# Optimization experiments

Measured on AMD Instinct MI355X. Metric: run time of the kernel, lower is better.

The kernel has to match this reference:

```python
import jax, jax.numpy as jnp
import numpy as np

N = 26000       # total nodes (1040 graphs * 25 joints)
E = 208000      # total edges
G = 1040        # graphs (16 samples * 65 frames)
FRAMES = 65
F_IN = 6
HID = 128
HEADS = 4
NCLS = 7


def setup_inputs() -> dict:
    key = jax.random.key(0)
    ks = jax.random.split(key, 30)

    def nrm(k, shape, s=0.05):
        return jax.random.normal(k, shape, dtype=jnp.float32) * s

    return {
        "x": jax.random.normal(ks[0], (N, F_IN), dtype=jnp.float32),
        "edge_index": jax.random.randint(ks[1], (2, E), 0, N, dtype=jnp.int32),
        "batch": jnp.arange(N, dtype=jnp.int32) // (N // G),  # 25 nodes per graph
        "w1_root": nrm(ks[2], (F_IN, HID)),
        "w1_nei": nrm(ks[3], (F_IN, HID)),
        "b1": nrm(ks[4], (HID,)),
        "wq": nrm(ks[5], (HID, HEADS * HID)),
        "bq": nrm(ks[6], (HEADS * HID,)),
        "wk": nrm(ks[7], (HID, HEADS * HID)),
        "bk": nrm(ks[8], (HEADS * HID,)),
        "wv": nrm(ks[9], (HID, HEADS * HID)),
        "bv": nrm(ks[10], (HEADS * HID,)),
        "wskip": nrm(ks[11], (HID, HEADS * HID)),
        "bskip": nrm(ks[12], (HEADS * HID,)),
        "skip_w": nrm(ks[13], (HID, HEADS * HID)),
        "lin1_w": nrm(ks[14], (HEADS * HID, HID)),
        "lin1_b": nrm(ks[15], (HID,)),
        "l2_root": nrm(ks[16], (HID, HID)),
        "l2_nei": nrm(ks[17], (HID, HID)),
        "l2_b": nrm(ks[18], (HID,)),
        "l3_root": nrm(ks[19], (HID, HID)),
        "l3_nei": nrm(ks[20], (HID, HID)),
        "l3_b": nrm(ks[21], (HID,)),
        "fc_w": nrm(ks[22], (HID, NCLS)),
        "fc_b": nrm(ks[23], (NCLS,)),
    }


def _graph_conv(x, src, dst, w_root, w_nei, b):
    # PyG GraphConv (aggr='add'): W_root x_i + W_nei * sum_{j in N(i)} x_j + b
    agg = jax.ops.segment_sum(x[src], dst, num_segments=N)
    return x @ w_root + agg @ w_nei + b


def _transformer_conv(x, src, dst, wq, bq, wk, bk, wv, bv, wskip, bskip):
    # PyG TransformerConv, concat=True, root_weight=True, beta=False.
    # Dropout on attention is inference-disabled.
    q = (x @ wq + bq).reshape(N, HEADS, HID)
    k = (x @ wk + bk).reshape(N, HEADS, HID)
    v = (x @ wv + bv).reshape(N, HEADS, HID)
    logits = jnp.einsum('ehc,ehc->eh', q[dst], k[src]) / jnp.sqrt(jnp.float32(HID))
    m = jax.ops.segment_max(logits, dst, num_segments=N)          # [N,H]
    a = jnp.exp(logits - m[dst])                                  # [E,H]
    denom = jax.ops.segment_sum(a, dst, num_segments=N)           # [N,H]
    num = jax.ops.segment_sum(a[:, :, None] * v[src], dst, num_segments=N)  # [N,H,C]
    out = num / jnp.where(denom == 0, 1.0, denom)[:, :, None]
    return out.reshape(N, HEADS * HID) + (x @ wskip + bskip)


def reference(x, edge_index, batch,
              w1_root, w1_nei, b1,
              wq, bq, wk, bk, wv, bv, wskip, bskip,
              skip_w, lin1_w, lin1_b,
              l2_root, l2_nei, l2_b,
              l3_root, l3_nei, l3_b,
              fc_w, fc_b):
    src, dst = edge_index[0], edge_index[1]
    h = jax.nn.relu(_graph_conv(x, src, dst, w1_root, w1_nei, b1))
    skip_out = h @ skip_w  # external skip Linear (no bias)
    h = jax.nn.relu(_transformer_conv(h, src, dst, wq, bq, wk, bk, wv, bv, wskip, bskip) + skip_out)
    h = jax.nn.relu(h @ lin1_w + lin1_b)
    for wr, wn, b in ((l2_root, l2_nei, l2_b), (l3_root, l3_nei, l3_b)):
        h = jax.nn.relu(_graph_conv(h, src, dst, wr, wn, b) + h)
    # global_mean_pool over graphs
    sums = jax.ops.segment_sum(h, batch, num_segments=G)
    cnts = jax.ops.segment_sum(jnp.ones((N,), jnp.float32), batch, num_segments=G)
    pooled = sums / jnp.where(cnts == 0, 1.0, cnts)[:, None]      # [G, HID]
    # average over 65 frames per sample, then classify
    z = pooled.reshape(-1, FRAMES, HID).mean(axis=1)              # [G/65, HID]
    return z @ fc_w + fc_b
```

## Files before the change

### kernel.cpp

```cpp
#include <hip/hip_runtime.h>
#include <math.h>

#define NN 26000
#define NE 208000
#define SCAN_CH 26

typedef __attribute__((ext_vector_type(8))) short bf16x8;
typedef __attribute__((ext_vector_type(4))) float f32x4;
typedef __attribute__((ext_vector_type(2))) float f32x2;
typedef unsigned char u8;

__device__ __forceinline__ float bf2f(ushort u){
  union { unsigned int i; float f; } w; w.i = ((unsigned int)u) << 16; return w.f;
}
__device__ __forceinline__ ushort f2bf(float f){
  union { float f; unsigned int i; } w; w.f = f;
  unsigned int u = w.i + 0x7fffu + ((w.i >> 16) & 1u);
  return (ushort)(u >> 16);
}

__global__ void count_k(const int* __restrict__ dst, int* __restrict__ cnt, int E){
  int e = blockIdx.x*256 + threadIdx.x;
  if (e < E) atomicAdd(&cnt[dst[e]], 1);
}

__global__ __launch_bounds__(1024) void scan_k(int* __restrict__ cnt_cur, int* __restrict__ off){
  int t = threadIdx.x;
  int base = t * SCAN_CH;
  int v[SCAN_CH];
  #pragma unroll
  for (int j = 0; j < SCAN_CH; ++j){
    int idx = base + j;
    v[j] = (idx < NN) ? cnt_cur[idx] : 0;
  }
  int s = 0;
  #pragma unroll
  for (int j = 0; j < SCAN_CH; ++j) s += v[j];
  __shared__ int ls[1024];
  ls[t] = s; __syncthreads();
  for (int ofs = 1; ofs < 1024; ofs <<= 1){
    int u = (t >= ofs) ? ls[t - ofs] : 0;
    __syncthreads();
    ls[t] += u;
    __syncthreads();
  }
  int run = (t == 0) ? 0 : ls[t-1];
  #pragma unroll
  for (int j = 0; j < SCAN_CH; ++j){
    int idx = base + j;
    if (idx < NN){
      off[idx] = run;
      cnt_cur[idx] = run;
      run += v[j];
    }
  }
  if (t == 1023) off[NN] = ls[1023];
}

__global__ void fill_k(const int* __restrict__ src, const int* __restrict__ dst,
                       int* __restrict__ cur, int* __restrict__ csrc, int E){
  int e = blockIdx.x*256 + threadIdx.x;
  if (e < E){
    int p = atomicAdd(&cur[dst[e]], 1);
    csrc[p] = src[e];
  }
}

__global__ __launch_bounds__(256) void layer1_k(
    const float* __restrict__ x, const int* __restrict__ off,
    const int* __restrict__ csrc, const float* __restrict__ w1r,
    const float* __restrict__ w1n, const float* __restrict__ b1,
    ushort* __restrict__ h1)
{
  __shared__ float aggs[2][6];
  int slot = threadIdx.x >> 7, c = threadIdx.x & 127;
  int i = blockIdx.x*2 + slot;
  if (c < 6){
    float s = 0.f;
    int e1 = off[i+1];
    for (int j = off[i]; j < e1; ++j) s += x[(size_t)csrc[j]*6 + c];
    aggs[slot][c] = s;
  }
  __syncthreads();
  float s = b1[c];
  #pragma unroll
  for (int f = 0; f < 6; ++f){
    s = fmaf(x[i*6+f],    w1r[f*128+c], s);
    s = fmaf(aggs[slot][f], w1n[f*128+c], s);
  }
  h1[(size_t)i*128 + c] = f2bf(fmaxf(s, 0.f));
}

__global__ void prep_w(const float* __restrict__ wq, const float* __restrict__ wk,
                       const float* __restrict__ wv, const float* __restrict__ wskip,
                       const float* __restrict__ skw, const float* __restrict__ lin1w,
                       const float* __restrict__ l2r, const float* __restrict__ l2n,
                       const float* __restrict__ l3r, const float* __restrict__ l3n,
                       ushort* __restrict__ wbuf){
  int idx = blockIdx.x*256 + threadIdx.x;
  if (idx >= 393216) return;
  float v;
  if (idx < 262144){
    int seg = idx >> 16;
    int local = idx & 65535;
    int n = local >> 7, kk = local & 127;
    const float* w = (seg == 0) ? wq : (seg == 1) ? wk : (seg == 2) ? wv : wskip;
    v = w[kk*512 + n];
    if (seg == 3) v += skw[kk*512 + n];
  } else if (idx < 327680){
    int local = idx - 262144;
    int n = local >> 9, kk = local & 511;
    v = lin1w[kk*128 + n];
  } else {
    int rem = idx - 327680;
    int seg = rem >> 14;
    int local = rem & 16383;
    int n = local >> 7, kk = local & 127;
    const float* w = (seg == 0) ? l2r : (seg == 1) ? l2n : (seg == 2) ? l3r : l3n;
    v = w[kk*128 + n];
  }
  wbuf[idx] = f2bf(v);
}

__global__ __launch_bounds__(256) void qkvs_k(
    const ushort* __restrict__ A, const ushort* __restrict__ BT,
    const float* __restrict__ bq, const float* __restrict__ bk,
    const float* __restrict__ bv, const float* __restrict__ bs,
    ushort* __restrict__ cq, u8* __restrict__ ckv,
    ushort* __restrict__ cs, int M)
{
  __shared__ ushort smem[2*128*72];
  ushort* Asm = smem;
  ushort* Bsm = smem + 128*72;
  int tid  = threadIdx.x;
  int lane = tid & 63;
  int wid  = tid >> 6;
  int wr = wid >> 1, wc = wid & 1;
  int rowbase = blockIdx.y * 128;
  int seg = blockIdx.x >> 2;
  const float* bias = (seg == 0) ? bq : (seg == 1) ? bk : (seg == 2) ? bv : bs;
  int colloc = (blockIdx.x & 3) * 128;
  int lr = lane & 15, lk = (lane >> 4) * 8;

  f32x4 acc[4][4] = {};

  for (int k0 = 0; k0 < 128; k0 += 64){
    #pragma unroll
    for (int i = 0; i < 4; ++i){
      int c = tid + i*256;
      int r = c >> 3, col8 = (c & 7) * 8;
      int row = rowbase + r;
      bf16x8 av = (bf16x8)0;
      if (row < M) av = *reinterpret_cast<const bf16x8*>(A + (size_t)row*128 + k0 + col8);
      *reinterpret_cast<bf16x8*>(&Asm[r*72 + col8]) = av;
      *reinterpret_cast<bf16x8*>(&Bsm[r*72 + col8]) =
          *reinterpret_cast<const bf16x8*>(BT + (size_t)(blockIdx.x*128 + r)*128 + k0 + col8);
    }
    __syncthreads();
    #pragma unroll
    for (int ks = 0; ks < 64; ks += 32){
      bf16x8 af[4], bfr[4];
      #pragma unroll
      for (int i = 0; i < 4; ++i)
        af[i] = *reinterpret_cast<const bf16x8*>(&Asm[(wr*64 + i*16 + lr)*72 + ks + lk]);
      #pragma unroll
      for (int j = 0; j < 4; ++j)
        bfr[j] = *reinterpret_cast<const bf16x8*>(&Bsm[(wc*64 + j*16 + lr)*72 + ks + lk]);
      #pragma unroll
      for (int i = 0; i < 4; ++i)
        #pragma unroll
        for (int j = 0; j < 4; ++j)
          acc[i][j] = __builtin_amdgcn_mfma_f32_16x16x32_bf16(af[i], bfr[j], acc[i][j], 0, 0, 0);
    }
    __syncthreads();
  }

  int rq = lane >> 4;
  if (seg == 1 || seg == 2){
    u8* tile = (u8*)smem;
    #pragma unroll
    for (int i = 0; i < 4; ++i)
      #pragma unroll
      for (int r = 0; r < 4; ++r){
        int lrow = wr*64 + i*16 + rq*4 + r;
        #pragma unroll
        for (int j = 0; j < 4; ++j){
          int lcol = wc*64 + j*16 + lr;
          float v = acc[i][j][r] + bias[colloc + lcol];
          unsigned int pk = __builtin_amdgcn_cvt_pk_fp8_f32(v, v, 0u, false);
          tile[lrow*136 + lcol] = (u8)(pk & 0xffu);
        }
      }
    __syncthreads();
    int cb = (seg == 1 ? 0 : 512) + colloc;
    #pragma unroll
    for (int t = tid; t < 2048; t += 256){
      int r = t >> 4, b8 = (t & 15) * 8;
      int row = rowbase + r;
      if (row < M)
        *reinterpret_cast<uint2*>(ckv + (size_t)row*1024 + cb + b8) =
            *reinterpret_cast<const uint2*>(&tile[r*136 + b8]);
    }
  } else {
    ushort* C = (seg == 0) ? cq : cs;
    #pragma unroll
    for (int i = 0; i < 4; ++i)
      #pragma unroll
      for (int r = 0; r < 4; ++r){
        int lrow = wr*64 + i*16 + rq*4 + r;
        #pragma unroll
        for (int j = 0; j < 4; ++j){
          int lcol = wc*64 + j*16 + lr;
          smem[lrow*136 + lcol] = f2bf(acc[i][j][r] + bias[colloc + lcol]);
        }
      }
    __syncthreads();
    #pragma unroll
    for (int t = tid; t < 2048; t += 256){
      int r = t >> 4, s8 = (t & 15) * 8;
      int row = rowbase + r;
      if (row < M)
        *reinterpret_cast<bf16x8*>(C + (size_t)row*512 + colloc + s8) =
            *reinterpret_cast<const bf16x8*>(&smem[r*136 + s8]);
    }
  }
}

template<bool RELU>
__global__ __launch_bounds__(256) void bgemm64_k(
    const ushort* __restrict__ A1, int lda1, const ushort* __restrict__ B1T, int K1,
    const float* __restrict__ bias, ushort* __restrict__ C, int M, int N)
{
  __shared__ ushort As[64][72];
  __shared__ ushort Bs[128][72];
  int tid  = threadIdx.x;
  int lane = tid & 63;
  int wid  = tid >> 6;
  int wr = wid >> 1, wc = wid & 1;
  int rowbase = blockIdx.y * 64;
  int colbase = blockIdx.x * 128;
  int lr = lane & 15, lk = (lane >> 4) * 8;

  f32x4 acc[2][4] = {};

  for (int k0 = 0; k0 < K1; k0 += 64){
    #pragma unroll
    for (int i = 0; i < 2; ++i){
      int c = tid + i*256;
      int r = c >> 3, col8 = (c & 7) * 8;
      int row = rowbase + r;
      bf16x8 av = (bf16x8)0;
      if (row < M) av = *reinterpret_cast<const bf16x8*>(A1 + (size_t)row*lda1 + k0 + col8);
      *reinterpret_cast<bf16x8*>(&As[r][col8]) = av;
    }
    #pragma unroll
    for (int i = 0; i < 4; ++i){
      int c = tid + i*256;
      int r = c >> 3, col8 = (c & 7) * 8;
      *reinterpret_cast<bf16x8*>(&Bs[r][col8]) =
          *reinterpret_cast<const bf16x8*>(B1T + (size_t)(colbase + r)*K1 + k0 + col8);
    }
    __syncthreads();
    #pragma unroll
    for (int ks = 0; ks < 64; ks += 32){
      bf16x8 af[2], bfr[4];
      #pragma unroll
      for (int i = 0; i < 2; ++i)
        af[i] = *reinterpret_cast<const bf16x8*>(&As[wr*32 + i*16 + lr][ks + lk]);
      #pragma unroll
      for (int j = 0; j < 4; ++j)
        bfr[j] = *reinterpret_cast<const bf16x8*>(&Bs[wc*64 + j*16 + lr][ks + lk]);
      #pragma unroll
      for (int i = 0; i < 2; ++i)
        #pragma unroll
        for (int j = 0; j < 4; ++j)
          acc[i][j] = __builtin_amdgcn_mfma_f32_16x16x32_bf16(af[i], bfr[j], acc[i][j], 0, 0, 0);
    }
    __syncthreads();
  }

  int rq = lane >> 4;
  #pragma unroll
  for (int i = 0; i < 2; ++i){
    #pragma unroll
    for (int r = 0; r < 4; ++r){
      int row = rowbase + wr*32 + i*16 + rq*4 + r;
      if (row >= M) continue;
      #pragma unroll
      for (int j = 0; j < 4; ++j){
        int col = colbase + wc*64 + j*16 + lr;
        if (col >= N) continue;
        float v = acc[i][j][r] + bias[col];
        if (RELU) v = fmaxf(v, 0.f);
        C[(size_t)row*N + col] = f2bf(v);
      }
    }
  }
}

__global__ __launch_bounds__(256) void gconv_k(
    const ushort* __restrict__ h, const ushort* __restrict__ WrT,
    const ushort* __restrict__ WnT, const float* __restrict__ bias,
    const int* __restrict__ off, const int* __restrict__ csrc,
    ushort* __restrict__ out, int M)
{
  __shared__ ushort As1[64][136];
  __shared__ ushort As2[64][136];
  __shared__ ushort Bs[128][72];
  int tid = threadIdx.x, lane = tid & 63, wid = tid >> 6;
  int wr = wid >> 1, wc = wid & 1;
  int rowbase = blockIdx.x * 64;
  int lr = lane & 15, lk = (lane >> 4) * 8;

  #pragma unroll
  for (int it = 0; it < 4; ++it){
    int c = tid + it*256;
    int r = c >> 4, col8 = (c & 15) * 8;
    int row = rowbase + r;
    bf16x8 av = (bf16x8)0;
    if (row < M) av = *reinterpret_cast<const bf16x8*>(h + (size_t)row*128 + col8);
    *reinterpret_cast<bf16x8*>(&As1[r][col8]) = av;
  }
  {
    int r = tid >> 2, sl = tid & 3;
    int row = rowbase + r;
    float a[32] = {};
    if (row < M){
      int e1 = off[row+1];
      for (int j = off[row]; j < e1; ++j){
        const ushort* hp = h + (size_t)csrc[j]*128 + sl*32;
        #pragma unroll
        for (int u = 0; u < 4; ++u){
          bf16x8 hv = *reinterpret_cast<const bf16x8*>(hp + u*8);
          #pragma unroll
          for (int p = 0; p < 8; ++p) a[u*8+p] += bf2f((ushort)hv[p]);
        }
      }
    }
    #pragma unroll
    for (int u = 0; u < 4; ++u){
      bf16x8 o;
      #pragma unroll
      for (int p = 0; p < 8; ++p) o[p] = (short)f2bf(a[u*8+p]);
      *reinterpret_cast<bf16x8*>(&As2[r][sl*32 + u*8]) = o;
    }
  }

  f32x4 acc[2][4] = {};
  #pragma unroll
  for (int pass = 0; pass < 2; ++pass){
    const ushort* BT = pass ? WnT : WrT;
    #pragma unroll
    for (int k0 = 0; k0 < 128; k0 += 64){
      __syncthreads();
      #pragma unroll
      for (int it = 0; it < 4; ++it){
        int c = tid + it*256;
        int r = c >> 3, col8 = (c & 7) * 8;
        *reinterpret_cast<bf16x8*>(&Bs[r][col8]) =
            *reinterpret_cast<const bf16x8*>(BT + (size_t)r*128 + k0 + col8);
      }
      __syncthreads();
      #pragma unroll
      for (int ks = 0; ks < 64; ks += 32){
        bf16x8 af[2], bfr[4];
        #pragma unroll
        for (int i = 0; i < 2; ++i)
          af[i] = pass
            ? *reinterpret_cast<const bf16x8*>(&As2[wr*32 + i*16 + lr][k0 + ks + lk])
            : *reinterpret_cast<const bf16x8*>(&As1[wr*32 + i*16 + lr][k0 + ks + lk]);
        #pragma unroll
        for (int j = 0; j < 4; ++j)
          bfr[j] = *reinterpret_cast<const bf16x8*>(&Bs[wc*64 + j*16 + lr][ks + lk]);
        #pragma unroll
        for (int i = 0; i < 2; ++i)
          #pragma unroll
          for (int j = 0; j < 4; ++j)
            acc[i][j] = __builtin_amdgcn_mfma_f32_16x16x32_bf16(af[i], bfr[j], acc[i][j], 0, 0, 0);
      }
    }
  }

  int rq = lane >> 4;
  #pragma unroll
  for (int i = 0; i < 2; ++i){
    #pragma unroll
    for (int r = 0; r < 4; ++r){
      int lrow = wr*32 + i*16 + rq*4 + r;
      int row = rowbase + lrow;
      if (row >= M) continue;
      #pragma unroll
      for (int j = 0; j < 4; ++j){
        int col = wc*64 + j*16 + lr;
        float v = acc[i][j][r] + bias[col] + bf2f(As1[lrow][col]);
        out[(size_t)row*128 + col] = f2bf(fmaxf(v, 0.f));
      }
    }
  }
}

__global__ __launch_bounds__(256) void attn_k(
    const ushort* __restrict__ q, const u8* __restrict__ kv,
    ushort* __restrict__ s_io,
    const int* __restrict__ off, const int* __restrict__ csrc)
{
  int lane = threadIdx.x & 63;
  int i = blockIdx.x*4 + (threadIdx.x >> 6);
  bf16x8 q8 = *reinterpret_cast<const bf16x8*>(q + (size_t)i*512 + lane*8);
  float qf[8];
  #pragma unroll
  for (int p = 0; p < 8; ++p) qf[p] = bf2f((ushort)q8[p]);

  float d = 0.f, acc[8] = {};
  int e0 = off[i], e1 = off[i+1];
  uint2 kA, vA, kB, vB;
  if (e0 < e1){
    const u8* r = kv + (size_t)csrc[e0]*1024 + lane*8;
    kA = *reinterpret_cast<const uint2*>(r);
    vA = *reinterpret_cast<const uint2*>(r + 512);
  }
  if (e0 + 1 < e1){
    const u8* r = kv + (size_t)csrc[e0+1]*1024 + lane*8;
    kB = *reinterpret_cast<const uint2*>(r);
    vB = *reinterpret_cast<const uint2*>(r + 512);
  }
  for (int j = e0; j < e1; ++j){
    uint2 kc = kA, vc = vA;
    kA = kB; vA = vB;
    if (j + 2 < e1){
      const u8* r = kv + (size_t)csrc[j+2]*1024 + lane*8;
      kB = *reinterpret_cast<const uint2*>(r);
      vB = *reinterpret_cast<const uint2*>(r + 512);
    }
    f32x2 k01 = __builtin_amdgcn_cvt_pk_f32_fp8(kc.x, false);
    f32x2 k23 = __builtin_amdgcn_cvt_pk_f32_fp8(kc.x, true);
    f32x2 k45 = __builtin_amdgcn_cvt_pk_f32_fp8(kc.y, false);
    f32x2 k67 = __builtin_amdgcn_cvt_pk_f32_fp8(kc.y, true);
    float t;
    t = qf[0] * k01[0];
    t = fmaf(qf[1], k01[1], t);
    t = fmaf(qf[2], k23[0], t);
    t = fmaf(qf[3], k23[1], t);
    t = fmaf(qf[4], k45[0], t);
    t = fmaf(qf[5], k45[1], t);
    t = fmaf(qf[6], k67[0], t);
    t = fmaf(qf[7], k67[1], t);
    t += __shfl_xor(t, 1);
    t += __shfl_xor(t, 2);
    t += __shfl_xor(t, 4);
    t += __shfl_xor(t, 8);
    float w = __expf(t * 0.08838834764831845f);
    d += w;
    f32x2 v01 = __builtin_amdgcn_cvt_pk_f32_fp8(vc.x, false);
    f32x2 v23 = __builtin_amdgcn_cvt_pk_f32_fp8(vc.x, true);
    f32x2 v45 = __builtin_amdgcn_cvt_pk_f32_fp8(vc.y, false);
    f32x2 v67 = __builtin_amdgcn_cvt_pk_f32_fp8(vc.y, true);
    acc[0] = fmaf(w, v01[0], acc[0]);
    acc[1] = fmaf(w, v01[1], acc[1]);
    acc[2] = fmaf(w, v23[0], acc[2]);
    acc[3] = fmaf(w, v23[1], acc[3]);
    acc[4] = fmaf(w, v45[0], acc[4]);
    acc[5] = fmaf(w, v45[1], acc[5]);
    acc[6] = fmaf(w, v67[0], acc[6]);
    acc[7] = fmaf(w, v67[1], acc[7]);
  }
  float inv = (d > 0.f) ? 1.f/d : 0.f;
  ushort* rowp = s_io + (size_t)i*512 + lane*8;
  bf16x8 sk8 = *reinterpret_cast<const bf16x8*>(rowp);
  bf16x8 o8;
  #pragma unroll
  for (int p = 0; p < 8; ++p)
    o8[p] = (short)f2bf(fmaxf(bf2f((ushort)sk8[p]) + acc[p]*inv, 0.f));
  *reinterpret_cast<bf16x8*>(rowp) = o8;
}

__global__ __launch_bounds__(256) void fc1_k(const ushort* __restrict__ h,
                                             float* __restrict__ partial){
  int s = blockIdx.x, c0 = blockIdx.y;
  int t = threadIdx.x;
  int c = t & 127, g = t >> 7;
  float sum = 0.f;
  int rend = (c0 + 1) * 125;
  for (int r = c0*125 + g; r < rend; r += 2)
    sum += bf2f(h[((size_t)s*1625 + r)*128 + c]);
  __shared__ float zs[2][128];
  zs[g][c] = sum; __syncthreads();
  if (g == 0) partial[((size_t)s*13 + c0)*128 + c] = zs[0][c] + zs[1][c];
}

__global__ __launch_bounds__(128) void fc2_k(const float* __restrict__ partial,
    const float* __restrict__ fcw, const float* __restrict__ fcb,
    float* __restrict__ out)
{
  int s = blockIdx.x;
  int c = threadIdx.x;
  float z = 0.f;
  #pragma unroll
  for (int p = 0; p < 13; ++p) z += partial[((size_t)s*13 + p)*128 + c];
  __shared__ float zs[128];
  zs[c] = z * (1.0f/1625.0f);
  __syncthreads();
  if (c < 7){
    float o = fcb[c];
    for (int k2 = 0; k2 < 128; ++k2) o = fmaf(zs[k2], fcw[k2*7 + c], o);
    out[s*7 + c] = o;
  }
}

extern "C" void kernel_launch(void* const* d_in, const int* in_sizes, int n_in,
                              void* d_out, int out_size, void* d_ws, size_t ws_size,
                              hipStream_t stream)
{
  const float* x     = (const float*)d_in[0];
  const int*   ei    = (const int*)  d_in[1];
  const float* w1r   = (const float*)d_in[3];
  const float* w1n   = (const float*)d_in[4];
  const float* b1    = (const float*)d_in[5];
  const float* wq    = (const float*)d_in[6];
  const float* bq    = (const float*)d_in[7];
  const float* wk    = (const float*)d_in[8];
  const float* bk    = (const float*)d_in[9];
  const float* wv    = (const float*)d_in[10];
  const float* bv    = (const float*)d_in[11];
  const float* wskip = (const float*)d_in[12];
  const float* bskip = (const float*)d_in[13];
  const float* skw   = (const float*)d_in[14];
  const float* lin1w = (const float*)d_in[15];
  const float* lin1b = (const float*)d_in[16];
  const float* l2r   = (const float*)d_in[17];
  const float* l2n   = (const float*)d_in[18];
  const float* l2b   = (const float*)d_in[19];
  const float* l3r   = (const float*)d_in[20];
  const float* l3n   = (const float*)d_in[21];
  const float* l3b   = (const float*)d_in[22];
  const float* fcw   = (const float*)d_in[23];
  const float* fcb   = (const float*)d_in[24];
  float* out = (float*)d_out;

  const int* src = ei;
  const int* dst = ei + NE;

  char* base = (char*)d_ws;
  size_t o = 0;
  auto alloc = [&](size_t bytes) -> void* {
    o = (o + 255) & ~(size_t)255;
    void* p = base + o; o += bytes; return p;
  };
  int*    cnt     = (int*)   alloc((size_t)NN*4);
  int*    off     = (int*)   alloc((size_t)(NN+1)*4);
  int*    csrc    = (int*)   alloc((size_t)NE*4);
  float*  partial = (float*) alloc((size_t)16*13*128*4);
  ushort* h1      = (ushort*)alloc((size_t)NN*128*2);
  ushort* wbuf    = (ushort*)alloc((size_t)393216*2);
  ushort* bufQ    = (ushort*)alloc((size_t)NN*512*2);
  u8*     bufKV   = (u8*)    alloc((size_t)NN*1024);
  ushort* bufS    = (ushort*)alloc((size_t)NN*512*2);
  (void)ws_size; (void)in_sizes; (void)n_in; (void)out_size;

  const ushort* lin1T = wbuf + 262144;
  const ushort* l2rT  = wbuf + 327680;
  const ushort* l2nT  = wbuf + 344064;
  const ushort* l3rT  = wbuf + 360448;
  const ushort* l3nT  = wbuf + 376832;

  ushort* h3 = bufQ;
  ushort* h4 = bufQ + (size_t)NN*128;
  ushort* h5 = bufS;

  hipMemsetAsync(cnt, 0, (size_t)NN*4, stream);
  count_k<<<(NE+255)/256, 256, 0, stream>>>(dst, cnt, NE);
  scan_k<<<1, 1024, 0, stream>>>(cnt, off);
  fill_k<<<(NE+255)/256, 256, 0, stream>>>(src, dst, cnt, csrc, NE);

  layer1_k<<<NN/2, 256, 0, stream>>>(x, off, csrc, w1r, w1n, b1, h1);

  prep_w<<<1536, 256, 0, stream>>>(wq, wk, wv, wskip, skw, lin1w, l2r, l2n, l3r, l3n, wbuf);

  {
    dim3 g(16, (NN+127)/128);
    qkvs_k<<<g, 256, 0, stream>>>(h1, wbuf, bq, bk, bv, bskip,
                                  bufQ, bufKV, bufS, NN);
  }

  attn_k<<<NN/4, 256, 0, stream>>>(bufQ, bufKV, bufS, off, csrc);

  {
    dim3 g(1, (NN+63)/64);
    bgemm64_k<true><<<g, 256, 0, stream>>>(
        bufS, 512, lin1T, 512, lin1b, h3, NN, 128);
  }

  gconv_k<<<(NN+63)/64, 256, 0, stream>>>(h3, l2rT, l2nT, l2b, off, csrc, h4, NN);
  gconv_k<<<(NN+63)/64, 256, 0, stream>>>(h4, l3rT, l3nT, l3b, off, csrc, h5, NN);

  {
    dim3 g1(16, 13);
    fc1_k<<<g1, 256, 0, stream>>>(h5, partial);
    fc2_k<<<16, 128, 0, stream>>>(partial, fcw, fcb, out);
  }
}
```

Baseline: 285.9 us.

## Store Q in FP8 and read GEMM weight fragments directly from global memory

The Q projection output is now written as FP8 instead of BF16, which halves the Q traffic read by the attention kernel; attention decodes it with packed fp8-to-f32 conversions. The qkvs, bgemm64 and gconv kernels no longer stage the B (weight) tile in shared memory. Each wave loads its B fragments straight from global memory, relying on cache hits, which cuts LDS use and barriers and should allow higher occupancy. The skip-output epilogue is written in two half-tile passes to fit the smaller shared buffer. In exchange Q loses precision, and the weights are now read redundantly from global memory.

```diff
diff --git a/kernel.cpp b/kernel.cpp
--- a/kernel.cpp
+++ b/kernel.cpp
@@ -126,12 +126,10 @@
     const ushort* __restrict__ A, const ushort* __restrict__ BT,
     const float* __restrict__ bq, const float* __restrict__ bk,
     const float* __restrict__ bv, const float* __restrict__ bs,
-    ushort* __restrict__ cq, u8* __restrict__ ckv,
+    u8* __restrict__ cq, u8* __restrict__ ckv,
     ushort* __restrict__ cs, int M)
 {
-  __shared__ ushort smem[2*128*72];
-  ushort* Asm = smem;
-  ushort* Bsm = smem + 128*72;
+  __shared__ ushort As[128][72];
   int tid  = threadIdx.x;
   int lane = tid & 63;
   int wid  = tid >> 6;
@@ -144,7 +142,9 @@
 
   f32x4 acc[4][4] = {};
 
+  #pragma unroll
   for (int k0 = 0; k0 < 128; k0 += 64){
+    __syncthreads();
     #pragma unroll
     for (int i = 0; i < 4; ++i){
       int c = tid + i*256;
@@ -152,9 +152,7 @@
       int row = rowbase + r;
       bf16x8 av = (bf16x8)0;
       if (row < M) av = *reinterpret_cast<const bf16x8*>(A + (size_t)row*128 + k0 + col8);
-      *reinterpret_cast<bf16x8*>(&Asm[r*72 + col8]) = av;
-      *reinterpret_cast<bf16x8*>(&Bsm[r*72 + col8]) =
-          *reinterpret_cast<const bf16x8*>(BT + (size_t)(blockIdx.x*128 + r)*128 + k0 + col8);
+      *reinterpret_cast<bf16x8*>(&As[r][col8]) = av;
     }
     __syncthreads();
     #pragma unroll
@@ -162,22 +160,23 @@
       bf16x8 af[4], bfr[4];
       #pragma unroll
       for (int i = 0; i < 4; ++i)
-        af[i] = *reinterpret_cast<const bf16x8*>(&Asm[(wr*64 + i*16 + lr)*72 + ks + lk]);
+        af[i] = *reinterpret_cast<const bf16x8*>(&As[wr*64 + i*16 + lr][ks + lk]);
       #pragma unroll
       for (int j = 0; j < 4; ++j)
-        bfr[j] = *reinterpret_cast<const bf16x8*>(&Bsm[(wc*64 + j*16 + lr)*72 + ks + lk]);
+        bfr[j] = *reinterpret_cast<const bf16x8*>(
+            BT + (size_t)(blockIdx.x*128 + wc*64 + j*16 + lr)*128 + k0 + ks + lk);
       #pragma unroll
       for (int i = 0; i < 4; ++i)
         #pragma unroll
         for (int j = 0; j < 4; ++j)
           acc[i][j] = __builtin_amdgcn_mfma_f32_16x16x32_bf16(af[i], bfr[j], acc[i][j], 0, 0, 0);
     }
-    __syncthreads();
   }
 
   int rq = lane >> 4;
-  if (seg == 1 || seg == 2){
-    u8* tile = (u8*)smem;
+  if (seg <= 2){
+    u8* tile = (u8*)&As[0][0];
+    __syncthreads();
     #pragma unroll
     for (int i = 0; i < 4; ++i)
       #pragma unroll
@@ -192,47 +191,53 @@
         }
       }
     __syncthreads();
-    int cb = (seg == 1 ? 0 : 512) + colloc;
+    u8* Cb; int ldb, cb;
+    if (seg == 0){ Cb = cq;  ldb = 512;  cb = colloc; }
+    else         { Cb = ckv; ldb = 1024; cb = (seg == 1 ? 0 : 512) + colloc; }
     #pragma unroll
     for (int t = tid; t < 2048; t += 256){
       int r = t >> 4, b8 = (t & 15) * 8;
       int row = rowbase + r;
       if (row < M)
-        *reinterpret_cast<uint2*>(ckv + (size_t)row*1024 + cb + b8) =
+        *reinterpret_cast<uint2*>(Cb + (size_t)row*ldb + cb + b8) =
             *reinterpret_cast<const uint2*>(&tile[r*136 + b8]);
     }
   } else {
-    ushort* C = (seg == 0) ? cq : cs;
-    #pragma unroll
-    for (int i = 0; i < 4; ++i)
-      #pragma unroll
-      for (int r = 0; r < 4; ++r){
-        int lrow = wr*64 + i*16 + rq*4 + r;
+    ushort* tile = &As[0][0];
+    #pragma unroll
+    for (int p = 0; p < 2; ++p){
+      __syncthreads();
+      if (wr == p){
         #pragma unroll
-        for (int j = 0; j < 4; ++j){
-          int lcol = wc*64 + j*16 + lr;
-          smem[lrow*136 + lcol] = f2bf(acc[i][j][r] + bias[colloc + lcol]);
-        }
+        for (int i = 0; i < 4; ++i)
+          #pragma unroll
+          for (int r = 0; r < 4; ++r){
+            int lrow = i*16 + rq*4 + r;
+            #pragma unroll
+            for (int j = 0; j < 4; ++j){
+              int lcol = wc*64 + j*16 + lr;
+              tile[lrow*136 + lcol] = f2bf(acc[i][j][r] + bias[colloc + lcol]);
+            }
+          }
       }
-    __syncthreads();
-    #pragma unroll
-    for (int t = tid; t < 2048; t += 256){
-      int r = t >> 4, s8 = (t & 15) * 8;
-      int row = rowbase + r;
-      if (row < M)
-        *reinterpret_cast<bf16x8*>(C + (size_t)row*512 + colloc + s8) =
-            *reinterpret_cast<const bf16x8*>(&smem[r*136 + s8]);
-    }
-  }
-}
-
-template<bool RELU>
+      __syncthreads();
+      #pragma unroll
+      for (int t = tid; t < 1024; t += 256){
+        int r = t >> 4, s8 = (t & 15) * 8;
+        int row = rowbase + p*64 + r;
+        if (row < M)
+          *reinterpret_cast<bf16x8*>(cs + (size_t)row*512 + colloc + s8) =
+              *reinterpret_cast<const bf16x8*>(&tile[r*136 + s8]);
+      }
+    }
+  }
+}
+
 __global__ __launch_bounds__(256) void bgemm64_k(
     const ushort* __restrict__ A1, int lda1, const ushort* __restrict__ B1T, int K1,
     const float* __restrict__ bias, ushort* __restrict__ C, int M, int N)
 {
   __shared__ ushort As[64][72];
-  __shared__ ushort Bs[128][72];
   int tid  = threadIdx.x;
   int lane = tid & 63;
   int wid  = tid >> 6;
@@ -244,6 +249,7 @@
   f32x4 acc[2][4] = {};
 
   for (int k0 = 0; k0 < K1; k0 += 64){
+    __syncthreads();
     #pragma unroll
     for (int i = 0; i < 2; ++i){
       int c = tid + i*256;
@@ -253,13 +259,6 @@
       if (row < M) av = *reinterpret_cast<const bf16x8*>(A1 + (size_t)row*lda1 + k0 + col8);
       *reinterpret_cast<bf16x8*>(&As[r][col8]) = av;
     }
-    #pragma unroll
-    for (int i = 0; i < 4; ++i){
-      int c = tid + i*256;
-      int r = c >> 3, col8 = (c & 7) * 8;
-      *reinterpret_cast<bf16x8*>(&Bs[r][col8]) =
-          *reinterpret_cast<const bf16x8*>(B1T + (size_t)(colbase + r)*K1 + k0 + col8);
-    }
     __syncthreads();
     #pragma unroll
     for (int ks = 0; ks < 64; ks += 32){
@@ -269,14 +268,14 @@
         af[i] = *reinterpret_cast<const bf16x8*>(&As[wr*32 + i*16 + lr][ks + lk]);
       #pragma unroll
       for (int j = 0; j < 4; ++j)
-        bfr[j] = *reinterpret_cast<const bf16x8*>(&Bs[wc*64 + j*16 + lr][ks + lk]);
+        bfr[j] = *reinterpret_cast<const bf16x8*>(
+            B1T + (size_t)(colbase + wc*64 + j*16 + lr)*K1 + k0 + ks + lk);
       #pragma unroll
       for (int i = 0; i < 2; ++i)
         #pragma unroll
         for (int j = 0; j < 4; ++j)
           acc[i][j] = __builtin_amdgcn_mfma_f32_16x16x32_bf16(af[i], bfr[j], acc[i][j], 0, 0, 0);
     }
-    __syncthreads();
   }
 
   int rq = lane >> 4;
@@ -290,8 +289,7 @@
       for (int j = 0; j < 4; ++j){
         int col = colbase + wc*64 + j*16 + lr;
         if (col >= N) continue;
-        float v = acc[i][j][r] + bias[col];
-        if (RELU) v = fmaxf(v, 0.f);
+        float v = fmaxf(acc[i][j][r] + bias[col], 0.f);
         C[(size_t)row*N + col] = f2bf(v);
       }
     }
@@ -306,7 +304,6 @@
 {
   __shared__ ushort As1[64][136];
   __shared__ ushort As2[64][136];
-  __shared__ ushort Bs[128][72];
   int tid = threadIdx.x, lane = tid & 63, wid = tid >> 6;
   int wr = wid >> 1, wc = wid & 1;
   int rowbase = blockIdx.x * 64;
@@ -345,39 +342,29 @@
       *reinterpret_cast<bf16x8*>(&As2[r][sl*32 + u*8]) = o;
     }
   }
+  __syncthreads();
 
   f32x4 acc[2][4] = {};
   #pragma unroll
   for (int pass = 0; pass < 2; ++pass){
     const ushort* BT = pass ? WnT : WrT;
     #pragma unroll
-    for (int k0 = 0; k0 < 128; k0 += 64){
-      __syncthreads();
-      #pragma unroll
-      for (int it = 0; it < 4; ++it){
-        int c = tid + it*256;
-        int r = c >> 3, col8 = (c & 7) * 8;
-        *reinterpret_cast<bf16x8*>(&Bs[r][col8]) =
-            *reinterpret_cast<const bf16x8*>(BT + (size_t)r*128 + k0 + col8);
-      }
-      __syncthreads();
-      #pragma unroll
-      for (int ks = 0; ks < 64; ks += 32){
-        bf16x8 af[2], bfr[4];
-        #pragma unroll
-        for (int i = 0; i < 2; ++i)
-          af[i] = pass
-            ? *reinterpret_cast<const bf16x8*>(&As2[wr*32 + i*16 + lr][k0 + ks + lk])
-            : *reinterpret_cast<const bf16x8*>(&As1[wr*32 + i*16 + lr][k0 + ks + lk]);
+    for (int kk = 0; kk < 128; kk += 32){
+      bf16x8 af[2], bfr[4];
+      #pragma unroll
+      for (int i = 0; i < 2; ++i)
+        af[i] = pass
+          ? *reinterpret_cast<const bf16x8*>(&As2[wr*32 + i*16 + lr][kk + lk])
+          : *reinterpret_cast<const bf16x8*>(&As1[wr*32 + i*16 + lr][kk + lk]);
+      #pragma unroll
+      for (int j = 0; j < 4; ++j)
+        bfr[j] = *reinterpret_cast<const bf16x8*>(
+            BT + (size_t)(wc*64 + j*16 + lr)*128 + kk + lk);
+      #pragma unroll
+      for (int i = 0; i < 2; ++i)
         #pragma unroll
         for (int j = 0; j < 4; ++j)
-          bfr[j] = *reinterpret_cast<const bf16x8*>(&Bs[wc*64 + j*16 + lr][ks + lk]);
-        #pragma unroll
-        for (int i = 0; i < 2; ++i)
-          #pragma unroll
-          for (int j = 0; j < 4; ++j)
-            acc[i][j] = __builtin_amdgcn_mfma_f32_16x16x32_bf16(af[i], bfr[j], acc[i][j], 0, 0, 0);
-      }
+          acc[i][j] = __builtin_amdgcn_mfma_f32_16x16x32_bf16(af[i], bfr[j], acc[i][j], 0, 0, 0);
     }
   }
 
@@ -400,16 +387,18 @@
 }
 
 __global__ __launch_bounds__(256) void attn_k(
-    const ushort* __restrict__ q, const u8* __restrict__ kv,
+    const u8* __restrict__ q, const u8* __restrict__ kv,
     ushort* __restrict__ s_io,
     const int* __restrict__ off, const int* __restrict__ csrc)
 {
   int lane = threadIdx.x & 63;
   int i = blockIdx.x*4 + (threadIdx.x >> 6);
-  bf16x8 q8 = *reinterpret_cast<const bf16x8*>(q + (size_t)i*512 + lane*8);
-  float qf[8];
-  #pragma unroll
-  for (int p = 0; p < 8; ++p) qf[p] = bf2f((ushort)q8[p]);
+  uint2 qv = *reinterpret_cast<const uint2*>(q + (size_t)i*512 + lane*8);
+  f32x2 q01 = __builtin_amdgcn_cvt_pk_f32_fp8(qv.x, false);
+  f32x2 q23 = __builtin_amdgcn_cvt_pk_f32_fp8(qv.x, true);
+  f32x2 q45 = __builtin_amdgcn_cvt_pk_f32_fp8(qv.y, false);
+  f32x2 q67 = __builtin_amdgcn_cvt_pk_f32_fp8(qv.y, true);
+  float qf[8] = {q01[0], q01[1], q23[0], q23[1], q45[0], q45[1], q67[0], q67[1]};
 
   float d = 0.f, acc[8] = {};
   int e0 = off[i], e1 = off[i+1];
@@ -552,9 +541,10 @@
   float*  partial = (float*) alloc((size_t)16*13*128*4);
   ushort* h1      = (ushort*)alloc((size_t)NN*128*2);
   ushort* wbuf    = (ushort*)alloc((size_t)393216*2);
-  ushort* bufQ    = (ushort*)alloc((size_t)NN*512*2);
+  u8*     bufQ8   = (u8*)    alloc((size_t)NN*512);
   u8*     bufKV   = (u8*)    alloc((size_t)NN*1024);
   ushort* bufS    = (ushort*)alloc((size_t)NN*512*2);
+  ushort* hbuf    = (ushort*)alloc((size_t)NN*256*2);
   (void)ws_size; (void)in_sizes; (void)n_in; (void)out_size;
 
   const ushort* lin1T = wbuf + 262144;
@@ -563,8 +553,8 @@
   const ushort* l3rT  = wbuf + 360448;
   const ushort* l3nT  = wbuf + 376832;
 
-  ushort* h3 = bufQ;
-  ushort* h4 = bufQ + (size_t)NN*128;
+  ushort* h3 = hbuf;
+  ushort* h4 = hbuf + (size_t)NN*128;
   ushort* h5 = bufS;
 
   hipMemsetAsync(cnt, 0, (size_t)NN*4, stream);
@@ -579,15 +569,14 @@
   {
     dim3 g(16, (NN+127)/128);
     qkvs_k<<<g, 256, 0, stream>>>(h1, wbuf, bq, bk, bv, bskip,
-                                  bufQ, bufKV, bufS, NN);
-  }
-
-  attn_k<<<NN/4, 256, 0, stream>>>(bufQ, bufKV, bufS, off, csrc);
+                                  bufQ8, bufKV, bufS, NN);
+  }
+
+  attn_k<<<NN/4, 256, 0, stream>>>(bufQ8, bufKV, bufS, off, csrc);
 
   {
     dim3 g(1, (NN+63)/64);
-    bgemm64_k<true><<<g, 256, 0, stream>>>(
-        bufS, 512, lin1T, 512, lin1b, h3, NN, 128);
+    bgemm64_k<<<g, 256, 0, stream>>>(bufS, 512, lin1T, 512, lin1b, h3, NN, 128);
   }
 
   gconv_k<<<(NN+63)/64, 256, 0, stream>>>(h3, l2rT, l2nT, l2b, off, csrc, h4, NN);
```

After: 304.6 us. 6.5% more time.
